# Performance work log

Hardware: AMD Instinct MI355X
Metric: run time of the kernel (lower is better)

The kernel has to match this reference:

```python
import jax, jax.numpy as jnp
import numpy as np

B, S, D, H = 2, 2048, 1024, 16
DH = D // H  # dim_per_head = 64


def setup_inputs() -> dict:
    key = jax.random.key(0)
    ks = jax.random.split(key, 12)
    std = 1.0 / np.sqrt(D)
    inp = {
        "key": jax.random.normal(ks[0], (B, S, D), jnp.float32),
        "value": jax.random.normal(ks[1], (B, S, D), jnp.float32),
        "query": jax.random.normal(ks[2], (B, S, D), jnp.float32),
        "mask": jax.random.randint(ks[3], (B, S, S), 0, 2) == 1,
        "Wk": jax.random.normal(ks[4], (D, D), jnp.float32) * std,
        "bk": jnp.zeros((D,), jnp.float32),
        "Wv": jax.random.normal(ks[5], (D, D), jnp.float32) * std,
        "bv": jnp.zeros((D,), jnp.float32),
        "Wq": jax.random.normal(ks[6], (D, D), jnp.float32) * std,
        "bq": jnp.zeros((D,), jnp.float32),
        "Wo": jax.random.normal(ks[7], (D, D), jnp.float32) * std,
        "bo": jnp.zeros((D,), jnp.float32),
    }
    return inp


def _shape(x):
    # (B, L, D) -> (B, H, L, DH)
    return x.reshape(B, -1, H, DH).transpose(0, 2, 1, 3)


def reference(key, value, query, mask, Wk, bk, Wv, bv, Wq, bq, Wo, bo):
    k = _shape(key @ Wk.T + bk)      # (B,H,S,DH)
    v = _shape(value @ Wv.T + bv)    # (B,H,S,DH)
    q = _shape(query @ Wq.T + bq)    # (B,H,S,DH)
    q = q / jnp.sqrt(jnp.asarray(DH, q.dtype))
    scores = jnp.einsum("bhqd,bhkd->bhqk", q, k).astype(jnp.float32)
    scores = jnp.where(mask[:, None, :, :], jnp.float32(-1e18), scores)
    attn = jax.nn.softmax(scores, axis=-1).astype(q.dtype)  # (B,H,S,S)
    # dropout p=0.0 -> identity
    ctx = jnp.einsum("bhqk,bhkd->bhqd", attn, v)
    ctx = ctx.transpose(0, 2, 1, 3).reshape(B, -1, D)
    output = ctx @ Wo.T + bo
    top_attn = attn[:, 0, :, :]
    return output, top_attn
```

## Files before the change

### kernel.cpp

```cpp
#include <hip/hip_runtime.h>

constexpr int BB = 2, SS = 2048, DD = 1024, HH = 16, DHH = 64;

typedef __attribute__((ext_vector_type(4))) float f32x4;
typedef __attribute__((ext_vector_type(8))) __bf16 bf16x8;
typedef __attribute__((ext_vector_type(8))) unsigned short us8;

__device__ __forceinline__ unsigned short f32_to_bf16(float f) {
    unsigned int u = __float_as_uint(f);
    u += 0x7fffu + ((u >> 16) & 1u);
    return (unsigned short)(u >> 16);
}

__device__ __forceinline__ ushort2 pk_bf16(float a, float b) {
#if __has_builtin(__builtin_amdgcn_cvt_pk_bf16_f32)
    typedef __attribute__((ext_vector_type(2))) __bf16 bf16x2;
    bf16x2 r = __builtin_amdgcn_cvt_pk_bf16_f32(a, b);
    return *(ushort2*)&r;
#else
    ushort2 r; r.x = f32_to_bf16(a); r.y = f32_to_bf16(b); return r;
#endif
}
__device__ __forceinline__ ushort4 pk_bf16x4(float a, float b, float c, float d) {
    const ushort2 lo = pk_bf16(a, b), hi = pk_bf16(c, d);
    ushort4 r; r.x = lo.x; r.y = lo.y; r.z = hi.x; r.w = hi.y;
    return r;
}

__device__ __forceinline__ f32x4 mfma_bf16(bf16x8 a, bf16x8 b, f32x4 c) {
    return __builtin_amdgcn_mfma_f32_16x16x32_bf16(a, b, c, 0, 0, 0);
}

__device__ __forceinline__ void stage16(const void* g, void* l) {
    typedef const __attribute__((address_space(1))) unsigned int gas_t;
    typedef __attribute__((address_space(3))) unsigned int las_t;
    __builtin_amdgcn_global_load_lds((gas_t*)(unsigned long long)g,
                                     (las_t*)(unsigned int)(unsigned long long)l,
                                     16, 0, 0);
}

__global__ __launch_bounds__(256) void cvt_bf16(const float* __restrict__ src,
                                                unsigned short* __restrict__ dst) {
    const size_t i = ((size_t)blockIdx.x * 256 + threadIdx.x) * 8;
    const float4 a = *(const float4*)(src + i);
    const float4 b = *(const float4*)(src + i + 4);
    ushort4 lo = pk_bf16x4(a.x, a.y, a.z, a.w);
    ushort4 hi = pk_bf16x4(b.x, b.y, b.z, b.w);
    us8 o;
    o[0] = lo.x; o[1] = lo.y; o[2] = lo.z; o[3] = lo.w;
    o[4] = hi.x; o[5] = hi.y; o[6] = hi.z; o[7] = hi.w;
    *(us8*)(dst + i) = o;
}

__global__ __launch_bounds__(256) void mask_pack(const int* __restrict__ mask,
                                                 unsigned long long* __restrict__ pm) {
    const int t = threadIdx.x;
    const size_t chunk = (size_t)blockIdx.x * 4 + (t >> 6);
    const int lane = t & 63;
    const int v = mask[chunk * 64 + lane];
    const unsigned long long b = __ballot(v != 0);
    if (lane == 0) pm[chunk] = b;
}

template <int MODE>
__global__ __launch_bounds__(256) void gemm_nt(const unsigned short* __restrict__ A,
                                               const unsigned short* __restrict__ Wb,
                                               const float* __restrict__ bias,
                                               void* __restrict__ outp,
                                               float scale) {
    constexpr int K = DD;
    __shared__ __align__(16) unsigned short Ash[128][72];
    __shared__ __align__(16) unsigned short Bsh[64][72];

    const int m0 = blockIdx.x * 128;
    const int n0 = blockIdx.y * 64;
    const int t = threadIdx.x;
    const int lane = t & 63, w = t >> 6;
    const int l15 = lane & 15, quad = lane >> 4;
    const int wm = (w >> 1) * 64, wn = (w & 1) * 32;

    f32x4 acc[4][2] = {};

    for (int k0 = 0; k0 < K; k0 += 64) {
        __syncthreads();
#pragma unroll
        for (int j = 0; j < 4; ++j) {
            const int v = t + j * 256;
            const int row = v >> 3, off = (v & 7) * 8;
            *(us8*)&Ash[row][off] = *(const us8*)&A[(size_t)(m0 + row) * K + k0 + off];
        }
#pragma unroll
        for (int j = 0; j < 2; ++j) {
            const int v = t + j * 256;
            const int row = v >> 3, off = (v & 7) * 8;
            *(us8*)&Bsh[row][off] = *(const us8*)&Wb[(size_t)(n0 + row) * K + k0 + off];
        }
        __syncthreads();

#pragma unroll
        for (int s = 0; s < 2; ++s) {
            bf16x8 af[4], bfr[2];
#pragma unroll
            for (int mi = 0; mi < 4; ++mi)
                af[mi] = *(const bf16x8*)&Ash[wm + mi * 16 + l15][s * 32 + quad * 8];
#pragma unroll
            for (int ni = 0; ni < 2; ++ni)
                bfr[ni] = *(const bf16x8*)&Bsh[wn + ni * 16 + l15][s * 32 + quad * 8];
#pragma unroll
            for (int mi = 0; mi < 4; ++mi)
#pragma unroll
                for (int ni = 0; ni < 2; ++ni)
                    acc[mi][ni] = mfma_bf16(af[mi], bfr[ni], acc[mi][ni]);
        }
    }

#pragma unroll
    for (int ni = 0; ni < 2; ++ni) {
        const int c = n0 + wn + ni * 16 + l15;
        const float bs = bias[c];
#pragma unroll
        for (int mi = 0; mi < 4; ++mi) {
#pragma unroll
            for (int r = 0; r < 4; ++r) {
                const int mrow = m0 + wm + mi * 16 + quad * 4 + r;
                const float val = (acc[mi][ni][r] + bs) * scale;
                if (MODE == 2) {
                    ((float*)outp)[(size_t)mrow * DD + c] = val;
                } else {
                    const int bi2 = mrow >> 11, si = mrow & (SS - 1);
                    const int hi2 = c >> 6, di = c & (DHH - 1);
                    unsigned short* o = (unsigned short*)outp;
                    if (MODE == 0)
                        o[((size_t)(bi2 * HH + hi2) * SS + si) * DHH + di] = f32_to_bf16(val);
                    else
                        o[((size_t)(bi2 * HH + hi2) * DHH + di) * SS + si] = f32_to_bf16(val);
                }
            }
        }
    }
}

__global__ __launch_bounds__(512, 4) void flash_attn(const unsigned short* __restrict__ qws,
                                                     const unsigned short* __restrict__ kws,
                                                     const unsigned short* __restrict__ vws,
                                                     const unsigned long long* __restrict__ pm,
                                                     unsigned short* __restrict__ ctx) {
    __shared__ __align__(16) unsigned short Ksh[2][64][64];
    __shared__ __align__(16) unsigned short Vsh[2][64][64];
    __shared__ __align__(16) unsigned short Psh[8][16][72];

    constexpr int NQT = SS / 128;
    const int qt = blockIdx.x % NQT;
    const int bh = blockIdx.x / NQT;
    const int bi = bh / HH, hi = bh % HH;

    const int t = threadIdx.x;
    const int lane = t & 63, w = t >> 6;
    const int l15 = lane & 15, quad = lane >> 4;
    const int sh4 = quad * 4;
    const int xk = quad ^ (l15 & 7);

    const unsigned short* qp = qws + (size_t)bh * SS * DHH;
    const unsigned short* kp = kws + (size_t)bh * SS * DHH;
    const unsigned short* vp = vws + (size_t)bh * DHH * SS;

    const int q_loc = qt * 128 + w * 16 + l15;
    const bf16x8 bq0 = *(const bf16x8*)(qp + (size_t)q_loc * DHH + quad * 8);
    const bf16x8 bq1 = *(const bf16x8*)(qp + (size_t)q_loc * DHH + 32 + quad * 8);
    const unsigned long long* pmrow = pm + ((size_t)bi * SS + q_loc) * (SS / 64);

    const int srow = lane >> 3;
    const int scol = (lane & 7) ^ srow;
    const unsigned short* kg = kp + (size_t)(w * 8 + srow) * DHH + scol * 8;
    const unsigned short* vg = vp + (size_t)(w * 8 + srow) * SS + scol * 8;

    f32x4 accO[4] = {};
    float m_run = -1e30f, l_run = 0.f;
    const float NEG_INF = -__builtin_inff();

    unsigned long long mcur = pmrow[0];
    stage16(kg, &Ksh[0][w * 8][0]);
    stage16(vg, &Vsh[0][w * 8][0]);

    constexpr int NT = SS / 64;
    for (int kt = 0; kt < NT; ++kt) {
        const int cur = kt & 1;
        unsigned long long mnxt = 0;
        if (kt < NT - 1) {
            mnxt = pmrow[kt + 1];
            stage16(kg + (size_t)(kt + 1) * 64 * DHH, &Ksh[cur ^ 1][w * 8][0]);
            stage16(vg + (size_t)(kt + 1) * 64,       &Vsh[cur ^ 1][w * 8][0]);
            __asm__ volatile("s_waitcnt vmcnt(3)" ::: "memory");
        } else {
            __asm__ volatile("s_waitcnt vmcnt(0)" ::: "memory");
        }
        __builtin_amdgcn_s_barrier();
        __builtin_amdgcn_sched_barrier(0);

        const unsigned short* Kb = &Ksh[cur][0][0];
        const unsigned short* Vb = &Vsh[cur][0][0];

        bf16x8 ak0[4], ak1[4];
#pragma unroll
        for (int i = 0; i < 4; ++i) {
            ak0[i] = *(const bf16x8*)&Kb[(i * 16 + l15) * 64 + xk * 8];
            ak1[i] = *(const bf16x8*)&Kb[(i * 16 + l15) * 64 + (xk ^ 4) * 8];
        }

        const unsigned int mlo = ((unsigned int)mcur) >> sh4;
        const unsigned int mhi = ((unsigned int)(mcur >> 32)) >> sh4;

        float sc[4][4];
        __builtin_amdgcn_s_setprio(1);
#pragma unroll
        for (int i = 0; i < 4; ++i) {
            f32x4 s4 = {};
            s4 = mfma_bf16(ak0[i], bq0, s4);
            s4 = mfma_bf16(ak1[i], bq1, s4);
            const unsigned int mw = (i & 2) ? mhi : mlo;
#pragma unroll
            for (int r = 0; r < 4; ++r)
                sc[i][r] = ((mw >> ((i & 1) * 16 + r)) & 1u) ? NEG_INF : s4[r];
        }
        __builtin_amdgcn_s_setprio(0);

        bf16x8 av0[4], av1[4];
#pragma unroll
        for (int i = 0; i < 4; ++i) {
            av0[i] = *(const bf16x8*)&Vb[(i * 16 + l15) * 64 + xk * 8];
            av1[i] = *(const bf16x8*)&Vb[(i * 16 + l15) * 64 + (xk ^ 4) * 8];
        }

        float tm = sc[0][0];
#pragma unroll
        for (int i = 0; i < 4; ++i)
#pragma unroll
            for (int r = 0; r < 4; ++r) tm = fmaxf(tm, sc[i][r]);
        tm = fmaxf(tm, __shfl_xor(tm, 16));
        tm = fmaxf(tm, __shfl_xor(tm, 32));
        const float mn = fmaxf(m_run, tm);
        const float alpha = __builtin_amdgcn_exp2f(m_run - mn);
        float rs = 0.f;
#pragma unroll
        for (int i = 0; i < 4; ++i)
#pragma unroll
            for (int r = 0; r < 4; ++r) {
                const float p = __builtin_amdgcn_exp2f(sc[i][r] - mn);
                sc[i][r] = p;
                rs += p;
            }
        rs += __shfl_xor(rs, 16);
        rs += __shfl_xor(rs, 32);
        l_run = l_run * alpha + rs;
        m_run = mn;
#pragma unroll
        for (int i = 0; i < 4; ++i) accO[i] *= alpha;

#pragma unroll
        for (int i = 0; i < 4; ++i)
            *(ushort4*)&Psh[w][l15][i * 16 + sh4] =
                pk_bf16x4(sc[i][0], sc[i][1], sc[i][2], sc[i][3]);
        __asm__ volatile("s_waitcnt lgkmcnt(0)" ::: "memory");

        const bf16x8 p0 = *(const bf16x8*)&Psh[w][l15][quad * 8];
        const bf16x8 p1 = *(const bf16x8*)&Psh[w][l15][32 + quad * 8];
        __builtin_amdgcn_s_setprio(1);
#pragma unroll
        for (int i = 0; i < 4; ++i) {
            accO[i] = mfma_bf16(av0[i], p0, accO[i]);
            accO[i] = mfma_bf16(av1[i], p1, accO[i]);
        }
        __builtin_amdgcn_s_setprio(0);

        __builtin_amdgcn_sched_barrier(0);
        __builtin_amdgcn_s_barrier();
        __builtin_amdgcn_sched_barrier(0);
        mcur = mnxt;
    }

    const float inv = 1.0f / l_run;
    unsigned short* cb = ctx + ((size_t)(bi * SS) + q_loc) * DD + hi * DHH;
#pragma unroll
    for (int i = 0; i < 4; ++i)
        *(ushort4*)&cb[i * 16 + sh4] = pk_bf16x4(accO[i][0] * inv, accO[i][1] * inv,
                                                 accO[i][2] * inv, accO[i][3] * inv);
}

__global__ __launch_bounds__(256) void score_h0(const unsigned short* __restrict__ q0,
                                                const unsigned short* __restrict__ k0,
                                                const unsigned long long* __restrict__ pm,
                                                float* __restrict__ outp,
                                                float2* __restrict__ stats) {
    __shared__ __align__(16) unsigned short Ksh[64][72];

    const int kc = blockIdx.x & 3;
    const int qt = (blockIdx.x >> 2) & 31;
    const int bi = blockIdx.x >> 7;

    const int t = threadIdx.x;
    const int lane = t & 63, w = t >> 6;
    const int l15 = lane & 15, quad = lane >> 4;
    const int sh4 = quad * 4;

    const int q = qt * 64 + w * 16 + l15;
    const unsigned short* qp = q0 + ((size_t)bi * SS + q) * DHH;
    const bf16x8 bq0 = *(const bf16x8*)(qp + quad * 8);
    const bf16x8 bq1 = *(const bf16x8*)(qp + 32 + quad * 8);

    const unsigned short* kp = k0 + (size_t)bi * SS * DHH;
    const unsigned long long* pmq = pm + ((size_t)bi * SS + q) * (SS / 64);
    float* orow = outp + ((size_t)bi * SS + q) * SS;

    float m_l = -1e30f, l_l = 0.f;

    for (int kt = 0; kt < 8; ++kt) {
        const int key0 = kc * 512 + kt * 64;
        __syncthreads();
#pragma unroll
        for (int hf = 0; hf < 2; ++hf) {
            const int v = t + hf * 256;
            const int row = v >> 3, off = (v & 7) * 8;
            *(us8*)&Ksh[row][off] = *(const us8*)(kp + (size_t)(key0 + row) * DHH + off);
        }
        __syncthreads();

        const unsigned long long m64 = pmq[kc * 8 + kt];
        const unsigned int mlo = ((unsigned int)m64) >> sh4;
        const unsigned int mhi = ((unsigned int)(m64 >> 32)) >> sh4;

        float sc[4][4];
        float lm = -1e30f;
#pragma unroll
        for (int i = 0; i < 4; ++i) {
            const bf16x8 ak0 = *(const bf16x8*)&Ksh[i * 16 + l15][quad * 8];
            const bf16x8 ak1 = *(const bf16x8*)&Ksh[i * 16 + l15][32 + quad * 8];
            f32x4 s4 = {};
            s4 = mfma_bf16(ak0, bq0, s4);
            s4 = mfma_bf16(ak1, bq1, s4);
            const unsigned int mw = (i & 2) ? mhi : mlo;
            float4 ov;
#pragma unroll
            for (int r = 0; r < 4; ++r) {
                const float s = ((mw >> ((i & 1) * 16 + r)) & 1u) ? -1e18f : s4[r];
                sc[i][r] = s;
                lm = fmaxf(lm, s);
            }
            ov.x = sc[i][0]; ov.y = sc[i][1]; ov.z = sc[i][2]; ov.w = sc[i][3];
            *(float4*)&orow[key0 + i * 16 + sh4] = ov;
        }

        const float mn = fmaxf(m_l, lm);
        float rs = 0.f;
#pragma unroll
        for (int i = 0; i < 4; ++i)
#pragma unroll
            for (int r = 0; r < 4; ++r) rs += __builtin_amdgcn_exp2f(sc[i][r] - mn);
        l_l = l_l * __builtin_amdgcn_exp2f(m_l - mn) + rs;
        m_l = mn;
    }

#pragma unroll
    for (int d = 16; d <= 32; d <<= 1) {
        const float mo = __shfl_xor(m_l, d);
        const float lo = __shfl_xor(l_l, d);
        const float mn = fmaxf(m_l, mo);
        l_l = l_l * __builtin_amdgcn_exp2f(m_l - mn) + lo * __builtin_amdgcn_exp2f(mo - mn);
        m_l = mn;
    }
    if (quad == 0) {
        float2 st; st.x = m_l; st.y = l_l;
        stats[((size_t)(bi * 4 + kc)) * SS + q] = st;
    }
}

__global__ __launch_bounds__(256) void scale_h0(float* __restrict__ scores,
                                                const float2* __restrict__ stats) {
    const int bi = blockIdx.x >> 11;
    const int si = blockIdx.x & (SS - 1);
    const int t = threadIdx.x;

    float M = -1e30f, L = 0.f;
#pragma unroll
    for (int c = 0; c < 4; ++c) {
        const float2 st = stats[((size_t)(bi * 4 + c)) * SS + si];
        const float mn = fmaxf(M, st.x);
        L = L * __builtin_amdgcn_exp2f(M - mn) + st.y * __builtin_amdgcn_exp2f(st.x - mn);
        M = mn;
    }
    const float inv = 1.0f / L;

    float* row = scores + (size_t)blockIdx.x * SS;
    const int base = t * 8;
    float4 a = *(const float4*)&row[base];
    float4 b = *(const float4*)&row[base + 4];
    a.x = __builtin_amdgcn_exp2f(a.x - M) * inv;
    a.y = __builtin_amdgcn_exp2f(a.y - M) * inv;
    a.z = __builtin_amdgcn_exp2f(a.z - M) * inv;
    a.w = __builtin_amdgcn_exp2f(a.w - M) * inv;
    b.x = __builtin_amdgcn_exp2f(b.x - M) * inv;
    b.y = __builtin_amdgcn_exp2f(b.y - M) * inv;
    b.z = __builtin_amdgcn_exp2f(b.z - M) * inv;
    b.w = __builtin_amdgcn_exp2f(b.w - M) * inv;
    *(float4*)&row[base] = a;
    *(float4*)&row[base + 4] = b;
}

extern "C" void kernel_launch(void* const* d_in, const int* in_sizes, int n_in,
                              void* d_out, int out_size, void* d_ws, size_t ws_size,
                              hipStream_t stream) {
    const float* key_   = (const float*)d_in[0];
    const float* value_ = (const float*)d_in[1];
    const float* query_ = (const float*)d_in[2];
    const int*   mask_  = (const int*)d_in[3];
    const float* Wk = (const float*)d_in[4];
    const float* bk = (const float*)d_in[5];
    const float* Wv = (const float*)d_in[6];
    const float* bv = (const float*)d_in[7];
    const float* Wq = (const float*)d_in[8];
    const float* bq = (const float*)d_in[9];
    const float* Wo = (const float*)d_in[10];
    const float* bo = (const float*)d_in[11];

    constexpr size_t XS  = (size_t)BB * SS * DD;
    constexpr size_t WSZ = (size_t)DD * DD;

    float* out_f = (float*)d_out;
    unsigned short* scratch = (unsigned short*)(out_f + XS);
    unsigned short* qws = scratch;
    unsigned short* kws = qws + XS;
    unsigned short* vws = kws + XS;
    unsigned short* ctx = vws + XS;

    unsigned short* q0 = (unsigned short*)d_ws;
    unsigned short* k0 = q0 + (size_t)BB * SS * DHH;
    unsigned long long* pm = (unsigned long long*)(k0 + (size_t)BB * SS * DHH);
    float2* stats = (float2*)(pm + (size_t)BB * SS * (SS / 64));

    unsigned short* Xq  = (unsigned short*)out_f;
    unsigned short* Xk  = Xq + XS;
    unsigned short* Xv  = kws;
    unsigned short* Wqb = ctx;
    unsigned short* Wkb = Wqb + WSZ;
    unsigned short* Wvb = Wkb + WSZ;
    unsigned short* Wob = qws;

    mask_pack<<<BB * SS * (SS / 64) / 4, 256, 0, stream>>>(mask_, pm);

    cvt_bf16<<<XS / 2048, 256, 0, stream>>>(query_, Xq);
    cvt_bf16<<<XS / 2048, 256, 0, stream>>>(key_,   Xk);
    cvt_bf16<<<XS / 2048, 256, 0, stream>>>(value_, Xv);
    cvt_bf16<<<WSZ / 2048, 256, 0, stream>>>(Wq, Wqb);
    cvt_bf16<<<WSZ / 2048, 256, 0, stream>>>(Wk, Wkb);
    cvt_bf16<<<WSZ / 2048, 256, 0, stream>>>(Wv, Wvb);

    const float qscale = 0.125f * 1.4426950408889634f;

    dim3 gg(BB * SS / 128, DD / 64);
    gemm_nt<0><<<gg, 256, 0, stream>>>(Xq, Wqb, bq, qws, qscale);
    gemm_nt<1><<<gg, 256, 0, stream>>>(Xv, Wvb, bv, vws, 1.0f);
    gemm_nt<0><<<gg, 256, 0, stream>>>(Xk, Wkb, bk, kws, 1.0f);

    for (int b = 0; b < BB; ++b) {
        hipMemcpyAsync(q0 + (size_t)b * SS * DHH, qws + (size_t)(b * HH) * SS * DHH,
                       (size_t)SS * DHH * sizeof(unsigned short),
                       hipMemcpyDeviceToDevice, stream);
        hipMemcpyAsync(k0 + (size_t)b * SS * DHH, kws + (size_t)(b * HH) * SS * DHH,
                       (size_t)SS * DHH * sizeof(unsigned short),
                       hipMemcpyDeviceToDevice, stream);
    }

    flash_attn<<<BB * HH * (SS / 128), 512, 0, stream>>>(qws, kws, vws, pm, ctx);

    cvt_bf16<<<WSZ / 2048, 256, 0, stream>>>(Wo, Wob);
    gemm_nt<2><<<gg, 256, 0, stream>>>(ctx, Wob, bo, out_f, 1.0f);

    score_h0<<<BB * 32 * 4, 256, 0, stream>>>(q0, k0, pm, out_f + XS, stats);
    scale_h0<<<BB * SS, 256, 0, stream>>>(out_f + XS, stats);
}
```

Before: 355.2 us.

## Double-buffer GEMM tiles with swizzled async staging and defer softmax rescaling

The projection GEMM now stages A and B tiles into two swizzled, unpadded LDS buffers using a stage16 helper. The next k-tile is prefetched while MFMAs run on the current one, with vmcnt waits and raw barriers instead of synchronous loads bracketed by __syncthreads. MFMA sections are also raised in priority. Separately, the attention softmax skips the running-max update and accumulator rescale when every lane's new tile max stays within 8 (log2 units) of the running max, which avoids exp and multiply work at the cost of a wave-wide vote and a slightly larger numerical range for the accumulated values.

```diff
diff --git a/kernel.cpp b/kernel.cpp
--- a/kernel.cpp
+++ b/kernel.cpp
@@ -69,8 +69,8 @@
                                                void* __restrict__ outp,
                                                float scale) {
     constexpr int K = DD;
-    __shared__ __align__(16) unsigned short Ash[128][72];
-    __shared__ __align__(16) unsigned short Bsh[64][72];
+    __shared__ __align__(16) unsigned short Ash[2][128][64];
+    __shared__ __align__(16) unsigned short Bsh[2][64][64];
 
     const int m0 = blockIdx.x * 128;
     const int n0 = blockIdx.y * 64;
@@ -79,39 +79,59 @@
     const int l15 = lane & 15, quad = lane >> 4;
     const int wm = (w >> 1) * 64, wn = (w & 1) * 32;
 
+    const int srow = lane >> 3;
+    const int scol8 = ((lane & 7) ^ srow) * 8;
+    const unsigned short* Ag = A + (size_t)(m0 + w * 32 + srow) * K + scol8;
+    const unsigned short* Bg = Wb + (size_t)(n0 + w * 16 + srow) * K + scol8;
+
     f32x4 acc[4][2] = {};
 
-    for (int k0 = 0; k0 < K; k0 += 64) {
-        __syncthreads();
-#pragma unroll
-        for (int j = 0; j < 4; ++j) {
-            const int v = t + j * 256;
-            const int row = v >> 3, off = (v & 7) * 8;
-            *(us8*)&Ash[row][off] = *(const us8*)&A[(size_t)(m0 + row) * K + k0 + off];
-        }
-#pragma unroll
-        for (int j = 0; j < 2; ++j) {
-            const int v = t + j * 256;
-            const int row = v >> 3, off = (v & 7) * 8;
-            *(us8*)&Bsh[row][off] = *(const us8*)&Wb[(size_t)(n0 + row) * K + k0 + off];
-        }
-        __syncthreads();
+#pragma unroll
+    for (int j = 0; j < 4; ++j) stage16(Ag + (size_t)j * 8 * K, &Ash[0][w * 32 + j * 8][0]);
+#pragma unroll
+    for (int j = 0; j < 2; ++j) stage16(Bg + (size_t)j * 8 * K, &Bsh[0][w * 16 + j * 8][0]);
+
+    for (int kk = 0; kk < K / 64; ++kk) {
+        const int cur = kk & 1;
+        if (kk < K / 64 - 1) {
+            const size_t ko = (size_t)(kk + 1) * 64;
+#pragma unroll
+            for (int j = 0; j < 4; ++j)
+                stage16(Ag + (size_t)j * 8 * K + ko, &Ash[cur ^ 1][w * 32 + j * 8][0]);
+#pragma unroll
+            for (int j = 0; j < 2; ++j)
+                stage16(Bg + (size_t)j * 8 * K + ko, &Bsh[cur ^ 1][w * 16 + j * 8][0]);
+            __asm__ volatile("s_waitcnt vmcnt(6)" ::: "memory");
+        } else {
+            __asm__ volatile("s_waitcnt vmcnt(0)" ::: "memory");
+        }
+        __builtin_amdgcn_s_barrier();
+        __builtin_amdgcn_sched_barrier(0);
+
+        const unsigned short* Ab = &Ash[cur][0][0];
+        const unsigned short* Bb = &Bsh[cur][0][0];
 
 #pragma unroll
         for (int s = 0; s < 2; ++s) {
+            const int ch = ((s * 4 + quad) ^ (l15 & 7)) * 8;
             bf16x8 af[4], bfr[2];
 #pragma unroll
             for (int mi = 0; mi < 4; ++mi)
-                af[mi] = *(const bf16x8*)&Ash[wm + mi * 16 + l15][s * 32 + quad * 8];
+                af[mi] = *(const bf16x8*)&Ab[(wm + mi * 16 + l15) * 64 + ch];
 #pragma unroll
             for (int ni = 0; ni < 2; ++ni)
-                bfr[ni] = *(const bf16x8*)&Bsh[wn + ni * 16 + l15][s * 32 + quad * 8];
+                bfr[ni] = *(const bf16x8*)&Bb[(wn + ni * 16 + l15) * 64 + ch];
+            __builtin_amdgcn_s_setprio(1);
 #pragma unroll
             for (int mi = 0; mi < 4; ++mi)
 #pragma unroll
                 for (int ni = 0; ni < 2; ++ni)
                     acc[mi][ni] = mfma_bf16(af[mi], bfr[ni], acc[mi][ni]);
-        }
+            __builtin_amdgcn_s_setprio(0);
+        }
+        __builtin_amdgcn_sched_barrier(0);
+        __builtin_amdgcn_s_barrier();
+        __builtin_amdgcn_sched_barrier(0);
     }
 
 #pragma unroll
@@ -238,8 +258,10 @@
             for (int r = 0; r < 4; ++r) tm = fmaxf(tm, sc[i][r]);
         tm = fmaxf(tm, __shfl_xor(tm, 16));
         tm = fmaxf(tm, __shfl_xor(tm, 32));
-        const float mn = fmaxf(m_run, tm);
-        const float alpha = __builtin_amdgcn_exp2f(m_run - mn);
+
+        const bool nodefer = !__all(tm <= m_run + 8.0f);
+        const float mn = nodefer ? fmaxf(m_run, tm) : m_run;
+
         float rs = 0.f;
 #pragma unroll
         for (int i = 0; i < 4; ++i)
@@ -251,10 +273,16 @@
             }
         rs += __shfl_xor(rs, 16);
         rs += __shfl_xor(rs, 32);
-        l_run = l_run * alpha + rs;
-        m_run = mn;
-#pragma unroll
-        for (int i = 0; i < 4; ++i) accO[i] *= alpha;
+
+        if (nodefer) {
+            const float alpha = __builtin_amdgcn_exp2f(m_run - mn);
+            l_run = l_run * alpha + rs;
+            m_run = mn;
+#pragma unroll
+            for (int i = 0; i < 4; ++i) accO[i] *= alpha;
+        } else {
+            l_run += rs;
+        }
 
 #pragma unroll
         for (int i = 0; i < 4; ++i)
```

After: 343.4 us. -3.3%, faster.
